# Optimization experiments

Measured on AMD Instinct MI355X. Metric: run time of the kernel, lower is better.

## Reference

```python
import jax, jax.numpy as jnp
import numpy as np

WS = 8      # window_size
C = 60      # channels
EXP = 2     # exp_ratio
DEPTH = 2   # 1 + shared_depth
B, H, W = 4, 256, 256
BN_EPS = 1e-5


def setup_inputs() -> dict:
    key = jax.random.key(0)
    ks = jax.random.split(key, 15)
    def rn(k, shape, s=0.1):
        return jax.random.normal(k, shape, jnp.float32) * s
    Ce = C * EXP
    return {
        "x": jax.random.normal(ks[0], (B, C, H, W), jnp.float32),
        "lfe_w0": rn(ks[1], (DEPTH, Ce, C)),
        "lfe_b0": rn(ks[2], (DEPTH, Ce)),
        "lfe_w1": rn(ks[3], (DEPTH, C, Ce)),
        "lfe_b1": rn(ks[4], (DEPTH, C)),
        "pi_w": rn(ks[5], (DEPTH, C, C)),
        "pi_b": rn(ks[6], (DEPTH, C)),
        "bn_g": 1.0 + rn(ks[7], (DEPTH, C)),
        "bn_b": rn(ks[8], (DEPTH, C)),
        "bn_m": rn(ks[9], (DEPTH, C)),
        "bn_v": jax.random.uniform(ks[10], (DEPTH, C), jnp.float32, 0.5, 1.5),
        "mask_w": rn(ks[11], (DEPTH, C, C)),
        "mask_b": rn(ks[12], (DEPTH, C)),
        "po_w": rn(ks[13], (DEPTH, C, C)),
        "po_b": rn(ks[14], (DEPTH, C)),
    }


def _conv1x1(x, w, b):
    # x: (b,c,h,w), w: (o,c)
    return jnp.einsum('oc,bchw->bohw', w, x) + b[None, :, None, None]


def _shift(x):
    # Faithful to ShiftConv2d1: depthwise 3x3 with one-hot kernels, zero pad=1.
    c = x.shape[1]; g = c // 5
    xp = jnp.pad(x, ((0, 0), (0, 0), (1, 1), (1, 1)))
    return jnp.concatenate([
        xp[:, 0 * g:1 * g, 1:-1, 2:],    # kernel (1,2): in[i, j+1]
        xp[:, 1 * g:2 * g, 1:-1, :-2],   # kernel (1,0): in[i, j-1]
        xp[:, 2 * g:3 * g, 2:, 1:-1],    # kernel (2,1): in[i+1, j]
        xp[:, 3 * g:4 * g, :-2, 1:-1],   # kernel (0,1): in[i-1, j]
        x[:, 4 * g:],                    # kernel (1,1): identity
    ], axis=1)


def _lfe(x, w0, b0, w1, b1):
    y = _conv1x1(_shift(x), w0, b0)
    y = jax.nn.gelu(y, approximate=False)  # torch nn.GELU() is exact erf
    return _conv1x1(_shift(y), w1, b1)


def _wsa(x, pi_w, pi_b, g, bt, m, v, mw, mb, pw, pb):
    b, c, h, w = x.shape; ws = WS
    # project_inp: 1x1 conv + BatchNorm2d (eval-mode stats)
    t = _conv1x1(x, pi_w, pi_b)
    scale = (g / jnp.sqrt(v + BN_EPS))
    t = (t - m[None, :, None, None]) * scale[None, :, None, None] + bt[None, :, None, None]
    # seq_refl_win_pad (forward): pad right/bottom by ws, then copy the
    # preceding ws-wide band into the padded region (rows first, then cols).
    xp = jnp.pad(t, ((0, 0), (0, 0), (0, ws), (0, ws)))
    xp = xp.at[:, :, -ws:, :].set(xp[:, :, -2 * ws:-ws, :])
    xp = xp.at[:, :, :, -ws:].set(xp[:, :, :, -2 * ws:-ws])
    nh, nw = h // ws, w // ws
    R = (jnp.arange(nh) * ws)[:, None] + jnp.arange(2 * ws)   # (nh, 2ws)
    Cc = (jnp.arange(nw) * ws)[:, None] + jnp.arange(2 * ws)  # (nw, 2ws)
    win = xp[:, :, R[:, None, :, None], Cc[None, :, None, :]]  # (b,c,nh,nw,2ws,2ws)
    # torch .unfold(3,..).unfold(2,..) yields window axes ordered (W-dir, H-dir)
    win = jnp.swapaxes(win, -1, -2)
    # 1x1 conv stride 2 == subsample every other pixel then 1x1 conv
    sub = win[..., ::2, ::2]  # (b,c,nh,nw,ws,ws)
    q = jnp.einsum('oc,bcijpq->bijpqo', mw, sub) + mb          # (b,nh,nw,ws,ws,c)
    q = q.reshape(b * nh * nw, ws * ws, c)
    vv = t.reshape(b, c, nh, ws, nw, ws).transpose(0, 2, 4, 3, 5, 1)
    vv = vv.reshape(b * nh * nw, ws * ws, c)
    atn = jax.nn.softmax(jnp.einsum('npc,nqc->npq', q, q), axis=-1)
    y = jnp.einsum('npq,nqc->npc', atn, vv)
    y = y.reshape(b, nh, nw, ws, ws, c).transpose(0, 5, 1, 3, 2, 4).reshape(b, c, h, w)
    return _conv1x1(y, pw, pb)


def reference(x, lfe_w0, lfe_b0, lfe_w1, lfe_b1, pi_w, pi_b, bn_g, bn_b, bn_m, bn_v, mask_w, mask_b, po_w, po_b):
    for i in range(DEPTH):
        x = _lfe(x, lfe_w0[i], lfe_b0[i], lfe_w1[i], lfe_b1[i]) + x
        x = _wsa(x, pi_w[i], pi_b[i], bn_g[i], bn_b[i], bn_m[i], bn_v[i],
                 mask_w[i], mask_b[i], po_w[i], po_b[i]) + x
    return x
```

## Files before the change

### kernel.cpp

```cpp
#include <hip/hip_runtime.h>
#include <math.h>

#define Hh 256
#define Ww 256
#define HW 65536
#define Bn 4
#define Cdim 60
#define Ce 120
#define NPIX (Bn*HW)

typedef const float* fp;

__device__ __forceinline__ float gelu_exact(float x){
  return 0.5f*x*(1.f + erff(x*0.70710678118654752f));
}

__device__ __forceinline__ void tile_decode(int blk, int& b, int& h, int& tw){
  b = blk >> 10; int rem = blk & 1023; h = rem >> 2; tw = (rem & 3) << 6;
}

__global__ __launch_bounds__(256) void k_lfe1(const float* __restrict__ X, float* __restrict__ Y1,
                                              fp w0, fp b0){
  __shared__ __align__(16) float A[60*64];
  __shared__ __align__(16) float Wn[120*61];
  int tid = threadIdx.x;
  int b, h, tw; tile_decode(blockIdx.x, b, h, tw);
  const float* Xb = X + (size_t)b*(Cdim*HW);
  for (int idx = tid; idx < 60*64; idx += 256){
    int k = idx >> 6, p = idx & 63;
    int grp = k / 12;
    int hh = h, ww = tw + p; bool ok = true;
    if (grp == 0){ ww += 1; ok = (ww < Ww); }
    else if (grp == 1){ ww -= 1; ok = (ww >= 0); }
    else if (grp == 2){ hh = h+1; ok = (hh < Hh); }
    else if (grp == 3){ hh = h-1; ok = (hh >= 0); }
    A[idx] = ok ? Xb[k*HW + hh*Ww + ww] : 0.f;
  }
  for (int idx = tid; idx < 120*60; idx += 256){
    int o = idx / 60, k = idx - o*60;
    Wn[o*61 + k] = w0[idx];
  }
  __syncthreads();
  if (tid < 240){
    int p0 = (tid & 15)*4;
    int o0 = (tid >> 4)*8;
    float acc[8][4];
    #pragma unroll
    for (int oi = 0; oi < 8; oi++){
      float bb = b0[o0+oi];
      #pragma unroll
      for (int pi = 0; pi < 4; pi++) acc[oi][pi] = bb;
    }
    #pragma unroll 4
    for (int k = 0; k < 60; k++){
      float4 a4 = *(const float4*)(&A[k*64 + p0]);
      float av[4] = {a4.x,a4.y,a4.z,a4.w};
      #pragma unroll
      for (int oi = 0; oi < 8; oi++){
        float wv = Wn[(o0+oi)*61 + k];
        #pragma unroll
        for (int pi = 0; pi < 4; pi++)
          acc[oi][pi] += wv*av[pi];
      }
    }
    float* Yb = Y1 + (size_t)b*(Ce*HW) + h*Ww + tw + p0;
    #pragma unroll
    for (int oi = 0; oi < 8; oi++){
      float4 r;
      r.x = gelu_exact(acc[oi][0]); r.y = gelu_exact(acc[oi][1]);
      r.z = gelu_exact(acc[oi][2]); r.w = gelu_exact(acc[oi][3]);
      *(float4*)(Yb + (size_t)(o0+oi)*HW) = r;
    }
  }
}

__global__ __launch_bounds__(256) void k_lfe2(const float* __restrict__ Y1,
                                              const float* __restrict__ R,
                                              float* __restrict__ X,
                                              fp w1, fp b1){
  __shared__ __align__(16) float A[60*64];
  __shared__ __align__(16) float Wn[60*121];
  int tid = threadIdx.x;
  int b, h, tw; tile_decode(blockIdx.x, b, h, tw);
  const float* Yb = Y1 + (size_t)b*(Ce*HW);
  for (int idx = tid; idx < 60*120; idx += 256){
    int c = idx / 120, e = idx - c*120;
    Wn[c*121 + e] = w1[idx];
  }
  int p0 = (tid & 15)*4;
  int o0 = (tid >> 4)*4;
  float acc[4][4];
  #pragma unroll
  for (int oi = 0; oi < 4; oi++)
    #pragma unroll
    for (int pi = 0; pi < 4; pi++) acc[oi][pi] = 0.f;
  #pragma unroll 1
  for (int half = 0; half < 2; half++){
    __syncthreads();
    for (int idx = tid; idx < 60*64; idx += 256){
      int k = idx >> 6, p = idx & 63;
      int e = half*60 + k;
      int grp = e / 24;
      int hh = h, ww = tw + p; bool ok = true;
      if (grp == 0){ ww += 1; ok = (ww < Ww); }
      else if (grp == 1){ ww -= 1; ok = (ww >= 0); }
      else if (grp == 2){ hh = h+1; ok = (hh < Hh); }
      else if (grp == 3){ hh = h-1; ok = (hh >= 0); }
      A[idx] = ok ? Yb[e*HW + hh*Ww + ww] : 0.f;
    }
    __syncthreads();
    if (tid < 240){
      #pragma unroll 4
      for (int k = 0; k < 60; k++){
        float4 a4 = *(const float4*)(&A[k*64 + p0]);
        float av[4] = {a4.x,a4.y,a4.z,a4.w};
        #pragma unroll
        for (int oi = 0; oi < 4; oi++){
          float wv = Wn[(o0+oi)*121 + half*60 + k];
          #pragma unroll
          for (int pi = 0; pi < 4; pi++)
            acc[oi][pi] += wv*av[pi];
        }
      }
    }
  }
  if (tid < 240){
    const float* Rp = R + (size_t)b*(Cdim*HW) + h*Ww + tw + p0;
    float* Xp = X + (size_t)b*(Cdim*HW) + h*Ww + tw + p0;
    #pragma unroll
    for (int oi = 0; oi < 4; oi++){
      int o = o0 + oi;
      float bb = b1[o];
      float4 r4 = *(const float4*)(Rp + (size_t)o*HW);
      float4 out;
      out.x = acc[oi][0] + bb + r4.x;
      out.y = acc[oi][1] + bb + r4.y;
      out.z = acc[oi][2] + bb + r4.z;
      out.w = acc[oi][3] + bb + r4.w;
      *(float4*)(Xp + (size_t)o*HW) = out;
    }
  }
}

__global__ __launch_bounds__(256) void k_wsat(const float* __restrict__ X, float* __restrict__ T,
                                              fp piw, fp pib, fp g, fp bt, fp m, fp v){
  __shared__ __align__(16) float A[60*64];
  __shared__ __align__(16) float Wn[60*61];
  int tid = threadIdx.x;
  int b, h, tw; tile_decode(blockIdx.x, b, h, tw);
  const float* Xb = X + (size_t)b*(Cdim*HW) + h*Ww + tw;
  for (int idx = tid; idx < 60*64; idx += 256){
    int k = idx >> 6, p = idx & 63;
    A[idx] = Xb[k*HW + p];
  }
  for (int idx = tid; idx < 60*60; idx += 256){
    int o = idx / 60, k = idx - o*60;
    float scale = g[o] * rsqrtf(v[o] + 1e-5f);
    Wn[o*61 + k] = piw[idx] * scale;
  }
  __syncthreads();
  if (tid < 240){
    int p0 = (tid & 15)*4;
    int o0 = (tid >> 4)*4;
    float acc[4][4];
    #pragma unroll
    for (int oi = 0; oi < 4; oi++)
      #pragma unroll
      for (int pi = 0; pi < 4; pi++) acc[oi][pi] = 0.f;
    #pragma unroll 4
    for (int k = 0; k < 60; k++){
      float4 a4 = *(const float4*)(&A[k*64 + p0]);
      float av[4] = {a4.x,a4.y,a4.z,a4.w};
      #pragma unroll
      for (int oi = 0; oi < 4; oi++){
        float wv = Wn[(o0+oi)*61 + k];
        #pragma unroll
        for (int pi = 0; pi < 4; pi++)
          acc[oi][pi] += wv*av[pi];
      }
    }
    float* Tb = T + (size_t)b*(Cdim*HW) + h*Ww + tw + p0;
    #pragma unroll
    for (int oi = 0; oi < 4; oi++){
      int o = o0 + oi;
      float scale = g[o] * rsqrtf(v[o] + 1e-5f);
      float cns   = (pib[o] - m[o])*scale + bt[o];
      float4 out;
      out.x = acc[oi][0] + cns;
      out.y = acc[oi][1] + cns;
      out.z = acc[oi][2] + cns;
      out.w = acc[oi][3] + cns;
      *(float4*)(Tb + (size_t)o*HW) = out;
    }
  }
}

__global__ __launch_bounds__(256) void k_attn(const float* __restrict__ T, float* __restrict__ Y,
                                              fp mw, fp mb){
  __shared__ __align__(16) float R1[64*68];
  __shared__ __align__(16) float R2[64*68];
  __shared__ __align__(16) float R3[60*64];
  int tid = threadIdx.x;
  int blk = blockIdx.x;
  int b = blk >> 10; int ij = blk & 1023; int wi = ij >> 5; int wj = ij & 31;
  const float* Tb = T + (size_t)b*(Cdim*HW);

  for (int idx = tid; idx < Cdim*64; idx += 256){
    int k = idx >> 6, p = idx & 63;
    int u = p >> 3, vq = p & 7;
    int r  = wi*8 + 2*vq; if (r > 255) r -= 8;
    int cc = wj*8 + 2*u;  if (cc > 255) cc -= 8;
    R1[k*68 + p] = Tb[k*HW + r*Ww + cc];
  }
  for (int idx = tid; idx < Cdim*Cdim; idx += 256){
    int c = idx / Cdim, k = idx - c*Cdim;
    R2[c*61 + k] = mw[idx];
  }
  __syncthreads();

  if (tid < 240){
    int p0 = (tid & 15)*4, c0 = (tid >> 4)*4;
    float4 mb4 = *(const float4*)(mb + c0);
    float bias[4] = {mb4.x, mb4.y, mb4.z, mb4.w};
    float acc[4][4];
    #pragma unroll
    for (int ci = 0; ci < 4; ci++)
      #pragma unroll
      for (int pi = 0; pi < 4; pi++) acc[ci][pi] = bias[ci];
    #pragma unroll 4
    for (int k = 0; k < Cdim; k++){
      float4 a4 = *(const float4*)(&R1[k*68 + p0]);
      float av[4] = {a4.x, a4.y, a4.z, a4.w};
      #pragma unroll
      for (int ci = 0; ci < 4; ci++){
        float wv = R2[(c0+ci)*61 + k];
        #pragma unroll
        for (int pi = 0; pi < 4; pi++)
          acc[ci][pi] += wv*av[pi];
      }
    }
    #pragma unroll
    for (int ci = 0; ci < 4; ci++)
      *(float4*)(&R3[(c0+ci)*64 + p0]) = make_float4(acc[ci][0], acc[ci][1], acc[ci][2], acc[ci][3]);
  }
  __syncthreads();

  {
    int p = tid & 63; int cg = tid >> 6;
    int pr = p >> 3, pc = p & 7;
    const float* base = Tb + (wi*8+pr)*Ww + (wj*8+pc);
    #pragma unroll
    for (int t2 = 0; t2 < 15; t2++)
      R1[p*68 + cg*15 + t2] = base[(cg*15+t2)*HW];
  }
  if (tid < 64){
    R1[tid*68 + 60] = 0.f; R1[tid*68 + 61] = 0.f;
    R1[tid*68 + 62] = 0.f; R1[tid*68 + 63] = 0.f;
  }
  {
    int p0 = (tid & 15)*4, q0 = (tid >> 4)*4;
    float acc[4][4];
    #pragma unroll
    for (int qi = 0; qi < 4; qi++)
      #pragma unroll
      for (int pi = 0; pi < 4; pi++) acc[qi][pi] = 0.f;
    #pragma unroll 4
    for (int c = 0; c < Cdim; c++){
      float4 A4 = *(const float4*)(&R3[c*64 + p0]);
      float4 B4 = *(const float4*)(&R3[c*64 + q0]);
      float Af[4] = {A4.x, A4.y, A4.z, A4.w};
      float Bf[4] = {B4.x, B4.y, B4.z, B4.w};
      #pragma unroll
      for (int qi = 0; qi < 4; qi++)
        #pragma unroll
        for (int pi = 0; pi < 4; pi++)
          acc[qi][pi] += Bf[qi]*Af[pi];
    }
    __syncthreads();
    #pragma unroll
    for (int qi = 0; qi < 4; qi++)
      *(float4*)(&R2[(q0+qi)*68 + p0]) = make_float4(acc[qi][0], acc[qi][1], acc[qi][2], acc[qi][3]);
  }
  __syncthreads();

  if (tid < 64){
    int p = tid;
    float mx = -1e30f;
    #pragma unroll
    for (int q = 0; q < 64; q++) mx = fmaxf(mx, R2[q*68 + p]);
    float sum = 0.f;
    #pragma unroll
    for (int q = 0; q < 64; q++){
      float e = __expf(R2[q*68 + p] - mx);
      R2[q*68 + p] = e; sum += e;
    }
    float inv = 1.f/sum;
    #pragma unroll
    for (int q = 0; q < 64; q++) R2[q*68 + p] *= inv;
  }
  __syncthreads();

  {
    int p0 = (tid & 15)*4, c0 = (tid >> 4)*4;
    float acc[4][4];
    #pragma unroll
    for (int ci = 0; ci < 4; ci++)
      #pragma unroll
      for (int pi = 0; pi < 4; pi++) acc[ci][pi] = 0.f;
    #pragma unroll 4
    for (int q = 0; q < 64; q++){
      float4 S4 = *(const float4*)(&R2[q*68 + p0]);
      float4 V4 = *(const float4*)(&R1[q*68 + c0]);
      float Sf[4] = {S4.x, S4.y, S4.z, S4.w};
      float Vf[4] = {V4.x, V4.y, V4.z, V4.w};
      #pragma unroll
      for (int ci = 0; ci < 4; ci++)
        #pragma unroll
        for (int pi = 0; pi < 4; pi++)
          acc[ci][pi] += Sf[pi]*Vf[ci];
    }
    float* Yb = Y + (size_t)b*(Cdim*HW);
    #pragma unroll
    for (int ci = 0; ci < 4; ci++){
      int c = c0 + ci;
      if (c < Cdim){
        #pragma unroll
        for (int pi = 0; pi < 4; pi++){
          int p = p0 + pi;
          Yb[c*HW + (wi*8 + (p>>3))*Ww + wj*8 + (p&7)] = acc[ci][pi];
        }
      }
    }
  }
}

__global__ __launch_bounds__(256) void k_wsaout(const float* __restrict__ Y, float* __restrict__ X,
                                                fp pw, fp pb){
  __shared__ __align__(16) float A[60*64];
  __shared__ __align__(16) float Wn[60*61];
  int tid = threadIdx.x;
  int b, h, tw; tile_decode(blockIdx.x, b, h, tw);
  const float* Yb = Y + (size_t)b*(Cdim*HW) + h*Ww + tw;
  for (int idx = tid; idx < 60*64; idx += 256){
    int k = idx >> 6, p = idx & 63;
    A[idx] = Yb[k*HW + p];
  }
  for (int idx = tid; idx < 60*60; idx += 256){
    int o = idx / 60, k = idx - o*60;
    Wn[o*61 + k] = pw[idx];
  }
  __syncthreads();
  if (tid < 240){
    int p0 = (tid & 15)*4;
    int o0 = (tid >> 4)*4;
    float acc[4][4];
    #pragma unroll
    for (int oi = 0; oi < 4; oi++)
      #pragma unroll
      for (int pi = 0; pi < 4; pi++) acc[oi][pi] = 0.f;
    #pragma unroll 4
    for (int k = 0; k < 60; k++){
      float4 a4 = *(const float4*)(&A[k*64 + p0]);
      float av[4] = {a4.x,a4.y,a4.z,a4.w};
      #pragma unroll
      for (int oi = 0; oi < 4; oi++){
        float wv = Wn[(o0+oi)*61 + k];
        #pragma unroll
        for (int pi = 0; pi < 4; pi++)
          acc[oi][pi] += wv*av[pi];
      }
    }
    float* Xp = X + (size_t)b*(Cdim*HW) + h*Ww + tw + p0;
    #pragma unroll
    for (int oi = 0; oi < 4; oi++){
      int o = o0 + oi;
      float bb = pb[o];
      float4 r4 = *(const float4*)(Xp + (size_t)o*HW);
      float4 out;
      out.x = acc[oi][0] + bb + r4.x;
      out.y = acc[oi][1] + bb + r4.y;
      out.z = acc[oi][2] + bb + r4.z;
      out.w = acc[oi][3] + bb + r4.w;
      *(float4*)(Xp + (size_t)o*HW) = out;
    }
  }
}

extern "C" void kernel_launch(void* const* d_in, const int* in_sizes, int n_in,
                              void* d_out, int out_size, void* d_ws, size_t ws_size,
                              hipStream_t stream){
  fp x      = (fp)d_in[0];
  fp lfe_w0 = (fp)d_in[1];
  fp lfe_b0 = (fp)d_in[2];
  fp lfe_w1 = (fp)d_in[3];
  fp lfe_b1 = (fp)d_in[4];
  fp pi_w   = (fp)d_in[5];
  fp pi_b   = (fp)d_in[6];
  fp bn_g   = (fp)d_in[7];
  fp bn_b   = (fp)d_in[8];
  fp bn_m   = (fp)d_in[9];
  fp bn_v   = (fp)d_in[10];
  fp mask_w = (fp)d_in[11];
  fp mask_b = (fp)d_in[12];
  fp po_w   = (fp)d_in[13];
  fp po_b   = (fp)d_in[14];

  const size_t XSZ = (size_t)Bn*Cdim*HW;
  float* X  = (float*)d_out;
  float* Y1 = (float*)d_ws;
  float* T  = Y1;
  float* Yw = Y1 + XSZ;

  const int NT = NPIX/64;

  for (int d = 0; d < 2; d++){
    fp src = (d == 0) ? x : X;
    k_lfe1  <<<NT, 256, 0, stream>>>(src, Y1, lfe_w0 + d*Ce*Cdim, lfe_b0 + d*Ce);
    k_lfe2  <<<NT, 256, 0, stream>>>(Y1, src, X, lfe_w1 + d*Ce*Cdim, lfe_b1 + d*Cdim);
    k_wsat  <<<NT, 256, 0, stream>>>(X, T, pi_w + d*Cdim*Cdim, pi_b + d*Cdim,
                                     bn_g + d*Cdim, bn_b + d*Cdim, bn_m + d*Cdim, bn_v + d*Cdim);
    k_attn  <<<Bn*32*32, 256, 0, stream>>>(T, Yw, mask_w + d*Cdim*Cdim, mask_b + d*Cdim);
    k_wsaout<<<NT, 256, 0, stream>>>(Yw, X, po_w + d*Cdim*Cdim, po_b + d*Cdim);
  }
}
```

Before: 1.092 ms.

## Read 1x1-conv weights as wave-uniform scalar loads instead of LDS-staged tiles

Restructures the four pointwise-conv kernels so each wavefront owns a slice of output channels and each lane one pixel. Weights are read directly from global memory with wave-uniform addresses (via readfirstlane), which can become scalar loads, and are no longer copied into LDS. This removes the per-block weight staging and cuts LDS usage, which together with explicit occupancy hints in launch_bounds should allow more resident blocks. In exchange, the stores become scalar per lane instead of float4, and the weight loads may not actually be promoted to scalar loads.

```diff
diff --git a/kernel.cpp b/kernel.cpp
--- a/kernel.cpp
+++ b/kernel.cpp
@@ -19,10 +19,9 @@
   b = blk >> 10; int rem = blk & 1023; h = rem >> 2; tw = (rem & 3) << 6;
 }
 
-__global__ __launch_bounds__(256) void k_lfe1(const float* __restrict__ X, float* __restrict__ Y1,
-                                              fp w0, fp b0){
+__global__ __launch_bounds__(256,3) void k_lfe1(const float* __restrict__ X, float* __restrict__ Y1,
+                                                fp w0, fp b0){
   __shared__ __align__(16) float A[60*64];
-  __shared__ __align__(16) float Wn[120*61];
   int tid = threadIdx.x;
   int b, h, tw; tile_decode(blockIdx.x, b, h, tw);
   const float* Xb = X + (size_t)b*(Cdim*HW);
@@ -36,64 +35,47 @@
     else if (grp == 3){ hh = h-1; ok = (hh >= 0); }
     A[idx] = ok ? Xb[k*HW + hh*Ww + ww] : 0.f;
   }
-  for (int idx = tid; idx < 120*60; idx += 256){
-    int o = idx / 60, k = idx - o*60;
-    Wn[o*61 + k] = w0[idx];
-  }
-  __syncthreads();
-  if (tid < 240){
-    int p0 = (tid & 15)*4;
-    int o0 = (tid >> 4)*8;
-    float acc[8][4];
-    #pragma unroll
-    for (int oi = 0; oi < 8; oi++){
-      float bb = b0[o0+oi];
-      #pragma unroll
-      for (int pi = 0; pi < 4; pi++) acc[oi][pi] = bb;
-    }
-    #pragma unroll 4
-    for (int k = 0; k < 60; k++){
-      float4 a4 = *(const float4*)(&A[k*64 + p0]);
-      float av[4] = {a4.x,a4.y,a4.z,a4.w};
-      #pragma unroll
-      for (int oi = 0; oi < 8; oi++){
-        float wv = Wn[(o0+oi)*61 + k];
-        #pragma unroll
-        for (int pi = 0; pi < 4; pi++)
-          acc[oi][pi] += wv*av[pi];
-      }
-    }
-    float* Yb = Y1 + (size_t)b*(Ce*HW) + h*Ww + tw + p0;
-    #pragma unroll
-    for (int oi = 0; oi < 8; oi++){
-      float4 r;
-      r.x = gelu_exact(acc[oi][0]); r.y = gelu_exact(acc[oi][1]);
-      r.z = gelu_exact(acc[oi][2]); r.w = gelu_exact(acc[oi][3]);
-      *(float4*)(Yb + (size_t)(o0+oi)*HW) = r;
-    }
-  }
-}
-
-__global__ __launch_bounds__(256) void k_lfe2(const float* __restrict__ Y1,
-                                              const float* __restrict__ R,
-                                              float* __restrict__ X,
-                                              fp w1, fp b1){
+  __syncthreads();
+  int lane = tid & 63;
+  int wid  = __builtin_amdgcn_readfirstlane(tid >> 6);
+  const float* Wd = w0 + wid*(30*60);
+  float acc[30];
+  #pragma unroll
+  for (int oi = 0; oi < 30; oi++) acc[oi] = 0.f;
+  #pragma unroll 2
+  for (int k = 0; k < 60; k += 4){
+    float a0 = A[(k+0)*64 + lane];
+    float a1 = A[(k+1)*64 + lane];
+    float a2 = A[(k+2)*64 + lane];
+    float a3 = A[(k+3)*64 + lane];
+    #pragma unroll
+    for (int oi = 0; oi < 30; oi++){
+      float4 w4 = *(const float4*)(Wd + oi*60 + k);
+      acc[oi] += w4.x*a0 + w4.y*a1 + w4.z*a2 + w4.w*a3;
+    }
+  }
+  float* Yb = Y1 + (size_t)b*(Ce*HW) + h*Ww + tw + lane;
+  #pragma unroll
+  for (int oi = 0; oi < 30; oi++){
+    int o = wid*30 + oi;
+    Yb[(size_t)o*HW] = gelu_exact(acc[oi] + b0[o]);
+  }
+}
+
+__global__ __launch_bounds__(256,4) void k_lfe2(const float* __restrict__ Y1,
+                                                const float* __restrict__ R,
+                                                float* __restrict__ X,
+                                                fp w1, fp b1){
   __shared__ __align__(16) float A[60*64];
-  __shared__ __align__(16) float Wn[60*121];
   int tid = threadIdx.x;
   int b, h, tw; tile_decode(blockIdx.x, b, h, tw);
   const float* Yb = Y1 + (size_t)b*(Ce*HW);
-  for (int idx = tid; idx < 60*120; idx += 256){
-    int c = idx / 120, e = idx - c*120;
-    Wn[c*121 + e] = w1[idx];
-  }
-  int p0 = (tid & 15)*4;
-  int o0 = (tid >> 4)*4;
-  float acc[4][4];
-  #pragma unroll
-  for (int oi = 0; oi < 4; oi++)
-    #pragma unroll
-    for (int pi = 0; pi < 4; pi++) acc[oi][pi] = 0.f;
+  int lane = tid & 63;
+  int wid  = __builtin_amdgcn_readfirstlane(tid >> 6);
+  const float* Wd = w1 + wid*(15*120);
+  float acc[15];
+  #pragma unroll
+  for (int oi = 0; oi < 15; oi++) acc[oi] = 0.f;
   #pragma unroll 1
   for (int half = 0; half < 2; half++){
     __syncthreads();
@@ -109,43 +91,31 @@
       A[idx] = ok ? Yb[e*HW + hh*Ww + ww] : 0.f;
     }
     __syncthreads();
-    if (tid < 240){
-      #pragma unroll 4
-      for (int k = 0; k < 60; k++){
-        float4 a4 = *(const float4*)(&A[k*64 + p0]);
-        float av[4] = {a4.x,a4.y,a4.z,a4.w};
-        #pragma unroll
-        for (int oi = 0; oi < 4; oi++){
-          float wv = Wn[(o0+oi)*121 + half*60 + k];
-          #pragma unroll
-          for (int pi = 0; pi < 4; pi++)
-            acc[oi][pi] += wv*av[pi];
-        }
+    #pragma unroll 2
+    for (int k = 0; k < 60; k += 4){
+      float a0 = A[(k+0)*64 + lane];
+      float a1 = A[(k+1)*64 + lane];
+      float a2 = A[(k+2)*64 + lane];
+      float a3 = A[(k+3)*64 + lane];
+      #pragma unroll
+      for (int oi = 0; oi < 15; oi++){
+        float4 w4 = *(const float4*)(Wd + oi*120 + half*60 + k);
+        acc[oi] += w4.x*a0 + w4.y*a1 + w4.z*a2 + w4.w*a3;
       }
     }
   }
-  if (tid < 240){
-    const float* Rp = R + (size_t)b*(Cdim*HW) + h*Ww + tw + p0;
-    float* Xp = X + (size_t)b*(Cdim*HW) + h*Ww + tw + p0;
-    #pragma unroll
-    for (int oi = 0; oi < 4; oi++){
-      int o = o0 + oi;
-      float bb = b1[o];
-      float4 r4 = *(const float4*)(Rp + (size_t)o*HW);
-      float4 out;
-      out.x = acc[oi][0] + bb + r4.x;
-      out.y = acc[oi][1] + bb + r4.y;
-      out.z = acc[oi][2] + bb + r4.z;
-      out.w = acc[oi][3] + bb + r4.w;
-      *(float4*)(Xp + (size_t)o*HW) = out;
-    }
-  }
-}
-
-__global__ __launch_bounds__(256) void k_wsat(const float* __restrict__ X, float* __restrict__ T,
-                                              fp piw, fp pib, fp g, fp bt, fp m, fp v){
+  const float* Rp = R + (size_t)b*(Cdim*HW) + h*Ww + tw + lane;
+  float* Xp = X + (size_t)b*(Cdim*HW) + h*Ww + tw + lane;
+  #pragma unroll
+  for (int oi = 0; oi < 15; oi++){
+    int o = wid*15 + oi;
+    Xp[(size_t)o*HW] = acc[oi] + b1[o] + Rp[(size_t)o*HW];
+  }
+}
+
+__global__ __launch_bounds__(256,4) void k_wsat(const float* __restrict__ X, float* __restrict__ T,
+                                                fp piw, fp pib, fp g, fp bt, fp m, fp v){
   __shared__ __align__(16) float A[60*64];
-  __shared__ __align__(16) float Wn[60*61];
   int tid = threadIdx.x;
   int b, h, tw; tile_decode(blockIdx.x, b, h, tw);
   const float* Xb = X + (size_t)b*(Cdim*HW) + h*Ww + tw;
@@ -153,45 +123,32 @@
     int k = idx >> 6, p = idx & 63;
     A[idx] = Xb[k*HW + p];
   }
-  for (int idx = tid; idx < 60*60; idx += 256){
-    int o = idx / 60, k = idx - o*60;
+  __syncthreads();
+  int lane = tid & 63;
+  int wid  = __builtin_amdgcn_readfirstlane(tid >> 6);
+  const float* Wd = piw + wid*(15*60);
+  float acc[15];
+  #pragma unroll
+  for (int oi = 0; oi < 15; oi++) acc[oi] = 0.f;
+  #pragma unroll 2
+  for (int k = 0; k < 60; k += 4){
+    float a0 = A[(k+0)*64 + lane];
+    float a1 = A[(k+1)*64 + lane];
+    float a2 = A[(k+2)*64 + lane];
+    float a3 = A[(k+3)*64 + lane];
+    #pragma unroll
+    for (int oi = 0; oi < 15; oi++){
+      float4 w4 = *(const float4*)(Wd + oi*60 + k);
+      acc[oi] += w4.x*a0 + w4.y*a1 + w4.z*a2 + w4.w*a3;
+    }
+  }
+  float* Tb = T + (size_t)b*(Cdim*HW) + h*Ww + tw + lane;
+  #pragma unroll
+  for (int oi = 0; oi < 15; oi++){
+    int o = wid*15 + oi;
     float scale = g[o] * rsqrtf(v[o] + 1e-5f);
-    Wn[o*61 + k] = piw[idx] * scale;
-  }
-  __syncthreads();
-  if (tid < 240){
-    int p0 = (tid & 15)*4;
-    int o0 = (tid >> 4)*4;
-    float acc[4][4];
-    #pragma unroll
-    for (int oi = 0; oi < 4; oi++)
-      #pragma unroll
-      for (int pi = 0; pi < 4; pi++) acc[oi][pi] = 0.f;
-    #pragma unroll 4
-    for (int k = 0; k < 60; k++){
-      float4 a4 = *(const float4*)(&A[k*64 + p0]);
-      float av[4] = {a4.x,a4.y,a4.z,a4.w};
-      #pragma unroll
-      for (int oi = 0; oi < 4; oi++){
-        float wv = Wn[(o0+oi)*61 + k];
-        #pragma unroll
-        for (int pi = 0; pi < 4; pi++)
-          acc[oi][pi] += wv*av[pi];
-      }
-    }
-    float* Tb = T + (size_t)b*(Cdim*HW) + h*Ww + tw + p0;
-    #pragma unroll
-    for (int oi = 0; oi < 4; oi++){
-      int o = o0 + oi;
-      float scale = g[o] * rsqrtf(v[o] + 1e-5f);
-      float cns   = (pib[o] - m[o])*scale + bt[o];
-      float4 out;
-      out.x = acc[oi][0] + cns;
-      out.y = acc[oi][1] + cns;
-      out.z = acc[oi][2] + cns;
-      out.w = acc[oi][3] + cns;
-      *(float4*)(Tb + (size_t)o*HW) = out;
-    }
+    float cns   = (pib[o] - m[o])*scale + bt[o];
+    Tb[(size_t)o*HW] = acc[oi]*scale + cns;
   }
 }
 
@@ -334,10 +291,9 @@
   }
 }
 
-__global__ __launch_bounds__(256) void k_wsaout(const float* __restrict__ Y, float* __restrict__ X,
-                                                fp pw, fp pb){
+__global__ __launch_bounds__(256,4) void k_wsaout(const float* __restrict__ Y, float* __restrict__ X,
+                                                  fp pw, fp pb){
   __shared__ __align__(16) float A[60*64];
-  __shared__ __align__(16) float Wn[60*61];
   int tid = threadIdx.x;
   int b, h, tw; tile_decode(blockIdx.x, b, h, tw);
   const float* Yb = Y + (size_t)b*(Cdim*HW) + h*Ww + tw;
@@ -345,44 +301,30 @@
     int k = idx >> 6, p = idx & 63;
     A[idx] = Yb[k*HW + p];
   }
-  for (int idx = tid; idx < 60*60; idx += 256){
-    int o = idx / 60, k = idx - o*60;
-    Wn[o*61 + k] = pw[idx];
-  }
-  __syncthreads();
-  if (tid < 240){
-    int p0 = (tid & 15)*4;
-    int o0 = (tid >> 4)*4;
-    float acc[4][4];
-    #pragma unroll
-    for (int oi = 0; oi < 4; oi++)
-      #pragma unroll
-      for (int pi = 0; pi < 4; pi++) acc[oi][pi] = 0.f;
-    #pragma unroll 4
-    for (int k = 0; k < 60; k++){
-      float4 a4 = *(const float4*)(&A[k*64 + p0]);
-      float av[4] = {a4.x,a4.y,a4.z,a4.w};
-      #pragma unroll
-      for (int oi = 0; oi < 4; oi++){
-        float wv = Wn[(o0+oi)*61 + k];
-        #pragma unroll
-        for (int pi = 0; pi < 4; pi++)
-          acc[oi][pi] += wv*av[pi];
-      }
-    }
-    float* Xp = X + (size_t)b*(Cdim*HW) + h*Ww + tw + p0;
-    #pragma unroll
-    for (int oi = 0; oi < 4; oi++){
-      int o = o0 + oi;
-      float bb = pb[o];
-      float4 r4 = *(const float4*)(Xp + (size_t)o*HW);
-      float4 out;
-      out.x = acc[oi][0] + bb + r4.x;
-      out.y = acc[oi][1] + bb + r4.y;
-      out.z = acc[oi][2] + bb + r4.z;
-      out.w = acc[oi][3] + bb + r4.w;
-      *(float4*)(Xp + (size_t)o*HW) = out;
-    }
+  __syncthreads();
+  int lane = tid & 63;
+  int wid  = __builtin_amdgcn_readfirstlane(tid >> 6);
+  const float* Wd = pw + wid*(15*60);
+  float acc[15];
+  #pragma unroll
+  for (int oi = 0; oi < 15; oi++) acc[oi] = 0.f;
+  #pragma unroll 2
+  for (int k = 0; k < 60; k += 4){
+    float a0 = A[(k+0)*64 + lane];
+    float a1 = A[(k+1)*64 + lane];
+    float a2 = A[(k+2)*64 + lane];
+    float a3 = A[(k+3)*64 + lane];
+    #pragma unroll
+    for (int oi = 0; oi < 15; oi++){
+      float4 w4 = *(const float4*)(Wd + oi*60 + k);
+      acc[oi] += w4.x*a0 + w4.y*a1 + w4.z*a2 + w4.w*a3;
+    }
+  }
+  float* Xp = X + (size_t)b*(Cdim*HW) + h*Ww + tw + lane;
+  #pragma unroll
+  for (int oi = 0; oi < 15; oi++){
+    int o = wid*15 + oi;
+    Xp[(size_t)o*HW] = acc[oi] + pb[o] + Xp[(size_t)o*HW];
   }
 }
 
```

New measurement: 1.143 ms. +4.7%, slower.
